# Kernel tuning notes

Hardware: AMD Instinct MI355X
Metric: run time of the kernel (lower is better)

Reference implementation:

```python
import jax, jax.numpy as jnp
import numpy as np

N_NODES = 50000


def gcn_conv(x, edge_index, W, b, n_nodes):
    # Linear transform first (as in PyG GCNConv), then normalized aggregation
    xw = x @ W  # [N, out]
    src, dst = edge_index[0], edge_index[1]
    loops = jnp.arange(n_nodes, dtype=src.dtype)
    s = jnp.concatenate([src, loops])  # add self-loops
    d = jnp.concatenate([dst, loops])
    deg = jax.ops.segment_sum(jnp.ones_like(s, dtype=xw.dtype), d, num_segments=n_nodes)
    dinv = jnp.where(deg > 0, jax.lax.rsqrt(deg), 0.0)
    norm = dinv[s] * dinv[d]  # [E+N]
    msg = xw[s] * norm[:, None]  # gather + scale
    out = jax.ops.segment_sum(msg, d, num_segments=n_nodes)  # scatter-add
    return out + b


def setup_inputs() -> dict:
    key = jax.random.key(0)
    k1, k2, k3, k4 = jax.random.split(key, 4)
    in_dim, hidden = 128, 128
    n_edges = 625000
    x = jax.random.normal(k1, (N_NODES, in_dim), dtype=jnp.float32)
    edge_index = jax.random.randint(k2, (2, n_edges), 0, N_NODES, dtype=jnp.int64)
    # glorot-ish scale
    W1 = jax.random.normal(k3, (in_dim, hidden), dtype=jnp.float32) * (1.0 / np.sqrt(in_dim))
    b1 = jnp.zeros((hidden,), dtype=jnp.float32)
    W2 = jax.random.normal(k4, (hidden, hidden), dtype=jnp.float32) * (1.0 / np.sqrt(hidden))
    b2 = jnp.zeros((hidden,), dtype=jnp.float32)
    return {"x": x, "edge_index": edge_index, "W1": W1, "b1": b1, "W2": W2, "b2": b2}


def reference(x, edge_index, W1, b1, W2, b2):
    n = x.shape[0]
    h = gcn_conv(x, edge_index, W1, b1, n)
    h = jax.nn.relu(h)
    # dropout(p=0.3) is identity in eval mode
    h = gcn_conv(h, edge_index, W2, b2, n)
    return jax.nn.relu(h)
```

## Files before the change

### kernel.cpp

```cpp
#include <hip/hip_runtime.h>
#include <hip/hip_bf16.h>

#define NNODES 50000
#define BKT 64
#define LP 136
#define EPT 8
#define AGG_BLOCKS 2048
#define AGE_BLOCKS 512

typedef short bf16x8 __attribute__((ext_vector_type(8)));
typedef float f32x4 __attribute__((ext_vector_type(4)));

__device__ __forceinline__ unsigned short f2bf_rn(float f) {
    unsigned int u = __float_as_uint(f);
    return (unsigned short)((u + 0x7fffu + ((u >> 16) & 1u)) >> 16);
}
__device__ __forceinline__ float bf_lo(unsigned int u) { return __uint_as_float(u << 16); }
__device__ __forceinline__ float bf_hi(unsigned int u) { return __uint_as_float(u & 0xffff0000u); }


__global__ __launch_bounds__(256) void k_wt(const float* __restrict__ W1,
                                            const float* __restrict__ W2,
                                            unsigned short* __restrict__ WT1,
                                            unsigned short* __restrict__ WT2,
                                            int* __restrict__ cnt, int N) {
    __shared__ float tile[128 * 129];
    int b = blockIdx.x, t = threadIdx.x;
    if (b < 2) {
        const float* W = b ? W2 : W1;
        unsigned short* WT = b ? WT2 : WT1;
        for (int idx = t; idx < 128 * 128; idx += 256)
            tile[(idx >> 7) * 129 + (idx & 127)] = W[idx];
        __syncthreads();
        for (int idx = t; idx < 128 * 128; idx += 256) {
            int c = idx >> 7, k = idx & 127;
            WT[c * 128 + k] = f2bf_rn(tile[k * 129 + c]);
        }
    } else {
        int i = (b - 2) * 256 + t;
        if (i < N) cnt[i] = 0;
    }
}


__device__ __forceinline__ void gather_accum(const unsigned int* __restrict__ xwb,
                                             const int* __restrict__ cnt,
                                             const unsigned short* __restrict__ bp,
                                             int degc, int lane,
                                             float& ax, float& ay) {
    float px = 0.f, py = 0.f;
    int j = 0;
    for (; j + 8 <= degc; j += 8) {
        int4 q = *(const int4*)&bp[j];
        int s0 = q.x & 0xffff, s1 = (int)((unsigned)q.x >> 16);
        int s2 = q.y & 0xffff, s3 = (int)((unsigned)q.y >> 16);
        int s4 = q.z & 0xffff, s5 = (int)((unsigned)q.z >> 16);
        int s6 = q.w & 0xffff, s7 = (int)((unsigned)q.w >> 16);
        unsigned int u0 = xwb[(size_t)s0 * 64 + lane];
        unsigned int u1 = xwb[(size_t)s1 * 64 + lane];
        unsigned int u2 = xwb[(size_t)s2 * 64 + lane];
        unsigned int u3 = xwb[(size_t)s3 * 64 + lane];
        unsigned int u4 = xwb[(size_t)s4 * 64 + lane];
        unsigned int u5 = xwb[(size_t)s5 * 64 + lane];
        unsigned int u6 = xwb[(size_t)s6 * 64 + lane];
        unsigned int u7 = xwb[(size_t)s7 * 64 + lane];
        float w0 = rsqrtf((float)cnt[s0] + 1.0f), w1 = rsqrtf((float)cnt[s1] + 1.0f);
        float w2 = rsqrtf((float)cnt[s2] + 1.0f), w3 = rsqrtf((float)cnt[s3] + 1.0f);
        float w4 = rsqrtf((float)cnt[s4] + 1.0f), w5 = rsqrtf((float)cnt[s5] + 1.0f);
        float w6 = rsqrtf((float)cnt[s6] + 1.0f), w7 = rsqrtf((float)cnt[s7] + 1.0f);
        ax = fmaf(bf_lo(u0), w0, ax);  ay = fmaf(bf_hi(u0), w0, ay);
        px = fmaf(bf_lo(u1), w1, px);  py = fmaf(bf_hi(u1), w1, py);
        ax = fmaf(bf_lo(u2), w2, ax);  ay = fmaf(bf_hi(u2), w2, ay);
        px = fmaf(bf_lo(u3), w3, px);  py = fmaf(bf_hi(u3), w3, py);
        ax = fmaf(bf_lo(u4), w4, ax);  ay = fmaf(bf_hi(u4), w4, ay);
        px = fmaf(bf_lo(u5), w5, px);  py = fmaf(bf_hi(u5), w5, py);
        ax = fmaf(bf_lo(u6), w6, ax);  ay = fmaf(bf_hi(u6), w6, ay);
        px = fmaf(bf_lo(u7), w7, px);  py = fmaf(bf_hi(u7), w7, py);
    }
    if (j + 4 <= degc) {
        int2 q = *(const int2*)&bp[j];
        int s0 = q.x & 0xffff, s1 = (int)((unsigned)q.x >> 16);
        int s2 = q.y & 0xffff, s3 = (int)((unsigned)q.y >> 16);
        unsigned int u0 = xwb[(size_t)s0 * 64 + lane];
        unsigned int u1 = xwb[(size_t)s1 * 64 + lane];
        unsigned int u2 = xwb[(size_t)s2 * 64 + lane];
        unsigned int u3 = xwb[(size_t)s3 * 64 + lane];
        float w0 = rsqrtf((float)cnt[s0] + 1.0f), w1 = rsqrtf((float)cnt[s1] + 1.0f);
        float w2 = rsqrtf((float)cnt[s2] + 1.0f), w3 = rsqrtf((float)cnt[s3] + 1.0f);
        ax = fmaf(bf_lo(u0), w0, ax);  ay = fmaf(bf_hi(u0), w0, ay);
        px = fmaf(bf_lo(u1), w1, px);  py = fmaf(bf_hi(u1), w1, py);
        ax = fmaf(bf_lo(u2), w2, ax);  ay = fmaf(bf_hi(u2), w2, ay);
        px = fmaf(bf_lo(u3), w3, px);  py = fmaf(bf_hi(u3), w3, py);
        j += 4;
    }
    for (; j < degc; ++j) {
        int s = bp[j];
        float wv = rsqrtf((float)cnt[s] + 1.0f);
        unsigned int u = xwb[(size_t)s * 64 + lane];
        ax = fmaf(bf_lo(u), wv, ax);
        ay = fmaf(bf_hi(u), wv, ay);
    }
    ax += px;
    ay += py;
}


__device__ __forceinline__ void gather_sum(const unsigned int* __restrict__ xwb,
                                           const unsigned short* __restrict__ bp,
                                           int degc, int lane,
                                           float& ax, float& ay) {
    float px = 0.f, py = 0.f;
    int j = 0;
    for (; j + 8 <= degc; j += 8) {
        int4 q = *(const int4*)&bp[j];
        int s0 = q.x & 0xffff, s1 = (int)((unsigned)q.x >> 16);
        int s2 = q.y & 0xffff, s3 = (int)((unsigned)q.y >> 16);
        int s4 = q.z & 0xffff, s5 = (int)((unsigned)q.z >> 16);
        int s6 = q.w & 0xffff, s7 = (int)((unsigned)q.w >> 16);
        unsigned int u0 = xwb[(size_t)s0 * 64 + lane];
        unsigned int u1 = xwb[(size_t)s1 * 64 + lane];
        unsigned int u2 = xwb[(size_t)s2 * 64 + lane];
        unsigned int u3 = xwb[(size_t)s3 * 64 + lane];
        unsigned int u4 = xwb[(size_t)s4 * 64 + lane];
        unsigned int u5 = xwb[(size_t)s5 * 64 + lane];
        unsigned int u6 = xwb[(size_t)s6 * 64 + lane];
        unsigned int u7 = xwb[(size_t)s7 * 64 + lane];
        ax += bf_lo(u0);  ay += bf_hi(u0);
        px += bf_lo(u1);  py += bf_hi(u1);
        ax += bf_lo(u2);  ay += bf_hi(u2);
        px += bf_lo(u3);  py += bf_hi(u3);
        ax += bf_lo(u4);  ay += bf_hi(u4);
        px += bf_lo(u5);  py += bf_hi(u5);
        ax += bf_lo(u6);  ay += bf_hi(u6);
        px += bf_lo(u7);  py += bf_hi(u7);
    }
    if (j + 4 <= degc) {
        int2 q = *(const int2*)&bp[j];
        int s0 = q.x & 0xffff, s1 = (int)((unsigned)q.x >> 16);
        int s2 = q.y & 0xffff, s3 = (int)((unsigned)q.y >> 16);
        unsigned int u0 = xwb[(size_t)s0 * 64 + lane];
        unsigned int u1 = xwb[(size_t)s1 * 64 + lane];
        unsigned int u2 = xwb[(size_t)s2 * 64 + lane];
        unsigned int u3 = xwb[(size_t)s3 * 64 + lane];
        ax += bf_lo(u0);  ay += bf_hi(u0);
        px += bf_lo(u1);  py += bf_hi(u1);
        ax += bf_lo(u2);  ay += bf_hi(u2);
        px += bf_lo(u3);  py += bf_hi(u3);
        j += 4;
    }
    for (; j < degc; ++j) {
        int s = bp[j];
        unsigned int u = xwb[(size_t)s * 64 + lane];
        ax += bf_lo(u);
        ay += bf_hi(u);
    }
    ax += px;
    ay += py;
}


__global__ __launch_bounds__(256) void k_gemmbucket(const float* __restrict__ X,
                                                    const unsigned short* __restrict__ WT,
                                                    unsigned short* __restrict__ Yb, int n,
                                                    const int* __restrict__ src,
                                                    const int* __restrict__ dst,
                                                    int* __restrict__ cnt,
                                                    unsigned short* __restrict__ bkt,
                                                    int E, int EB8) {
    __shared__ unsigned short Ep[64 * LP];
    int t = threadIdx.x;
    int b = blockIdx.x;
    int region = EB8 * 3;
    if (b < region && (b % 3) == 0) {
        int bid = b / 3;
        int e0 = bid * 256 * EPT + t * EPT;
        if (e0 + EPT <= E) {
            int4 sa = *(const int4*)&src[e0];
            int4 sb = *(const int4*)&src[e0 + 4];
            int4 da = *(const int4*)&dst[e0];
            int4 db = *(const int4*)&dst[e0 + 4];
            int p;
            p = atomicAdd(&cnt[da.x], 1); if (p < BKT) bkt[(size_t)da.x * BKT + p] = (unsigned short)sa.x;
            p = atomicAdd(&cnt[da.y], 1); if (p < BKT) bkt[(size_t)da.y * BKT + p] = (unsigned short)sa.y;
            p = atomicAdd(&cnt[da.z], 1); if (p < BKT) bkt[(size_t)da.z * BKT + p] = (unsigned short)sa.z;
            p = atomicAdd(&cnt[da.w], 1); if (p < BKT) bkt[(size_t)da.w * BKT + p] = (unsigned short)sa.w;
            p = atomicAdd(&cnt[db.x], 1); if (p < BKT) bkt[(size_t)db.x * BKT + p] = (unsigned short)sb.x;
            p = atomicAdd(&cnt[db.y], 1); if (p < BKT) bkt[(size_t)db.y * BKT + p] = (unsigned short)sb.y;
            p = atomicAdd(&cnt[db.z], 1); if (p < BKT) bkt[(size_t)db.z * BKT + p] = (unsigned short)sb.z;
            p = atomicAdd(&cnt[db.w], 1); if (p < BKT) bkt[(size_t)db.w * BKT + p] = (unsigned short)sb.w;
        } else {
#pragma unroll
            for (int k = 0; k < EPT; ++k) {
                int e = e0 + k;
                if (e < E) {
                    int s = src[e], d = dst[e];
                    int pos = atomicAdd(&cnt[d], 1);
                    if (pos < BKT) bkt[(size_t)d * BKT + pos] = (unsigned short)s;
                }
            }
        }
        return;
    }
    int gb = (b < region) ? (b - (b + 2) / 3) : (b - EB8);
    int lane = t & 63, w = t >> 6;
    int m = lane & 15, quad = lane >> 4;
    int base = gb * 64 + w * 16;
    int row = min(base + m, n - 1);

    bf16x8 a[4];
#pragma unroll
    for (int kt = 0; kt < 4; ++kt) {
        const float* pa = &X[(size_t)row * 128 + kt * 32 + quad * 8];
        float4 v0 = *(const float4*)pa;
        float4 v1 = *(const float4*)(pa + 4);
        a[kt][0] = (short)f2bf_rn(v0.x); a[kt][1] = (short)f2bf_rn(v0.y);
        a[kt][2] = (short)f2bf_rn(v0.z); a[kt][3] = (short)f2bf_rn(v0.w);
        a[kt][4] = (short)f2bf_rn(v1.x); a[kt][5] = (short)f2bf_rn(v1.y);
        a[kt][6] = (short)f2bf_rn(v1.z); a[kt][7] = (short)f2bf_rn(v1.w);
    }

    f32x4 acc[8];
#pragma unroll
    for (int i = 0; i < 8; ++i) acc[i] = f32x4{0.f, 0.f, 0.f, 0.f};
#pragma unroll
    for (int kt = 0; kt < 4; ++kt) {
        int ko = kt * 32 + quad * 8;
#pragma unroll
        for (int ct = 0; ct < 8; ++ct) {
            bf16x8 bfrag = *(const bf16x8*)&WT[(ct * 16 + m) * 128 + ko];
            acc[ct] = __builtin_amdgcn_mfma_f32_16x16x32_bf16(a[kt], bfrag, acc[ct], 0, 0, 0);
        }
    }

    unsigned short* ep = &Ep[w * 16 * LP];
#pragma unroll
    for (int ct = 0; ct < 8; ++ct)
#pragma unroll
        for (int r = 0; r < 4; ++r)
            ep[(quad * 4 + r) * LP + ct * 16 + m] = f2bf_rn(acc[ct][r]);
    __syncthreads();
    int rr = lane & 15, cc = lane >> 4;
    int orow = base + rr;
    if (orow < n) {
#pragma unroll
        for (int i2 = 0; i2 < 4; ++i2)
            ((uint4*)&Yb[(size_t)orow * 128])[cc * 4 + i2] =
                *(const uint4*)&ep[rr * LP + (cc * 4 + i2) * 8];
    }
}


__global__ __launch_bounds__(1024, 2) void k_aggemm(const unsigned int* __restrict__ xw1,
                                                    const int* __restrict__ cnt,
                                                    const unsigned short* __restrict__ bkt,
                                                    const float* __restrict__ bias,
                                                    const unsigned short* __restrict__ WT2,
                                                    unsigned short* __restrict__ xw2,
                                                    int n, int ntiles) {
    __shared__ unsigned short At[16 * LP];
    __shared__ float dis[16];
    int t = threadIdx.x, lane = t & 63, w = t >> 6;
    int m = lane & 15, quad = lane >> 4;
    float bx = bias[lane * 2], by = bias[lane * 2 + 1];

    for (int tile = blockIdx.x; tile < ntiles; tile += gridDim.x) {
        int base = tile * 16;
        int i = min(base + w, n - 1);
        int deg = cnt[i];
        int degc = min(deg, BKT);
        float di = rsqrtf((float)deg + 1.0f);
        unsigned int v0 = xw1[(size_t)i * 64 + lane];
        float ax = di * bf_lo(v0), ay = di * bf_hi(v0);
        gather_accum(xw1, cnt, &bkt[(size_t)i * BKT], degc, lane, ax, ay);
        ax = fmaxf(fmaf(di, ax, bx), 0.0f);
        ay = fmaxf(fmaf(di, ay, by), 0.0f);
        ((unsigned int*)&At[w * LP])[lane] =
            (unsigned)f2bf_rn(ax) | ((unsigned)f2bf_rn(ay) << 16);
        if (lane == 0) dis[w] = di;
        __syncthreads();

        f32x4 acc = f32x4{0.f, 0.f, 0.f, 0.f};
        if (w < 8) {
            bf16x8 a[4];
#pragma unroll
            for (int kt = 0; kt < 4; ++kt)
                a[kt] = *(const bf16x8*)&At[m * LP + kt * 32 + quad * 8];
#pragma unroll
            for (int kt = 0; kt < 4; ++kt) {
                bf16x8 bfrag = *(const bf16x8*)&WT2[(w * 16 + m) * 128 + kt * 32 + quad * 8];
                acc = __builtin_amdgcn_mfma_f32_16x16x32_bf16(a[kt], bfrag, acc, 0, 0, 0);
            }
        }
        __syncthreads();
        if (w < 8) {
#pragma unroll
            for (int r = 0; r < 4; ++r)
                At[(quad * 4 + r) * LP + w * 16 + m] = f2bf_rn(acc[r] * dis[quad * 4 + r]);
        }
        __syncthreads();
        if (t < 256) {
            int row = t >> 4, q = t & 15;
            int orow = base + row;
            if (orow < n)
                *(uint4*)&xw2[(size_t)orow * 128 + q * 8] =
                    *(const uint4*)&At[row * LP + q * 8];
        }
        __syncthreads();
    }
}


__global__ __launch_bounds__(256) void k_agg(const unsigned int* __restrict__ xwb,
                                             const int* __restrict__ cnt,
                                             const unsigned short* __restrict__ bkt,
                                             const float* __restrict__ bias,
                                             float* __restrict__ out, int n) {
    int lane = threadIdx.x & 63;
    int gw = (blockIdx.x * 256 + threadIdx.x) >> 6;
    int nw = (gridDim.x * 256) >> 6;
    float bx = bias[lane * 2], by = bias[lane * 2 + 1];
    for (int i = gw; i < n; i += nw) {
        int deg = cnt[i];
        int degc = min(deg, BKT);
        float di = rsqrtf((float)deg + 1.0f);
        unsigned int v0 = xwb[(size_t)i * 64 + lane];
        float ax = bf_lo(v0), ay = bf_hi(v0);
        gather_sum(xwb, &bkt[(size_t)i * BKT], degc, lane, ax, ay);
        ax = fmaxf(fmaf(di, ax, bx), 0.0f);
        ay = fmaxf(fmaf(di, ay, by), 0.0f);
        ((float2*)out)[(size_t)i * 64 + lane] = make_float2(ax, ay);
    }
}


extern "C" void kernel_launch(void* const* d_in, const int* in_sizes, int n_in,
                              void* d_out, int out_size, void* d_ws, size_t ws_size,
                              hipStream_t stream) {
    const float* x  = (const float*)d_in[0];
    const int*   ei = (const int*)d_in[1];
    const float* W1 = (const float*)d_in[2];
    const float* b1 = (const float*)d_in[3];
    const float* W2 = (const float*)d_in[4];
    const float* b2 = (const float*)d_in[5];
    float* out = (float*)d_out;

    const int N = NNODES;
    const int E = in_sizes[1] / 2;
    const int* src = ei;
    const int* dst = ei + E;

    char* p = (char*)d_ws;
    size_t off = 0;
    auto take = [&](size_t bytes) -> void* {
        void* r = p + off;
        off = (off + bytes + 255) & ~(size_t)255;
        return r;
    };
    int* cnt = (int*)take((size_t)N * 4);
    unsigned short* bkt = (unsigned short*)take((size_t)N * BKT * 2);
    unsigned short* w1t = (unsigned short*)take(128 * 128 * 2);
    unsigned short* w2t = (unsigned short*)take(128 * 128 * 2);
    unsigned short* xw1 = (unsigned short*)take((size_t)N * 128 * 2);
    unsigned short* xw2 = (unsigned short*)take((size_t)N * 128 * 2);

    const int NB = (N + 255) / 256;
    const int EB8 = (E + 256 * EPT - 1) / (256 * EPT);
    const int GB = (N + 63) / 64;
    const int NT = (N + 15) / 16;

    k_wt<<<2 + NB, 256, 0, stream>>>(W1, W2, w1t, w2t, cnt, N);
    k_gemmbucket<<<EB8 + GB, 256, 0, stream>>>(x, w1t, xw1, N, src, dst, cnt, bkt, E, EB8);
    k_aggemm<<<AGE_BLOCKS, 1024, 0, stream>>>((const unsigned int*)xw1, cnt, bkt,
                                              b1, w2t, xw2, N, NT);
    k_agg<<<AGG_BLOCKS, 256, 0, stream>>>((const unsigned int*)xw2, cnt, bkt,
                                          b2, out, N);
}
```

Measured before the change: 219.4 us.

## Restructure fused aggregate-GEMM to per-wave 16-row tiles with LDS-staged W2

The fused layer-1 aggregation plus layer-2 GEMM kernel now has each wave aggregate 16 nodes into its own LDS tile, then run a full 16x128 MFMA product against W2, which is staged once per block in LDS. Before, a 1024-thread persistent block synchronised three times per 16-node tile, left half its waves idle during the GEMM, and read W2 fragments from global memory. The new layout drops all block-wide barriers in the main loop and raises MFMA work per wave. In exchange it uses about 52KB of LDS per block, which may limit occupancy, and holds more accumulator registers.

```diff
diff --git a/kernel.cpp b/kernel.cpp
--- a/kernel.cpp
+++ b/kernel.cpp
@@ -6,7 +6,6 @@
 #define LP 136
 #define EPT 8
 #define AGG_BLOCKS 2048
-#define AGE_BLOCKS 512
 
 typedef short bf16x8 __attribute__((ext_vector_type(8)));
 typedef float f32x4 __attribute__((ext_vector_type(4)));
@@ -250,22 +249,30 @@
 }
 
 
-__global__ __launch_bounds__(1024, 2) void k_aggemm(const unsigned int* __restrict__ xw1,
-                                                    const int* __restrict__ cnt,
-                                                    const unsigned short* __restrict__ bkt,
-                                                    const float* __restrict__ bias,
-                                                    const unsigned short* __restrict__ WT2,
-                                                    unsigned short* __restrict__ xw2,
-                                                    int n, int ntiles) {
-    __shared__ unsigned short At[16 * LP];
-    __shared__ float dis[16];
+__global__ __launch_bounds__(256) void k_aggemm(const unsigned int* __restrict__ xw1,
+                                                const int* __restrict__ cnt,
+                                                const unsigned short* __restrict__ bkt,
+                                                const float* __restrict__ bias,
+                                                const unsigned short* __restrict__ WT2,
+                                                unsigned short* __restrict__ xw2, int n) {
+    __shared__ unsigned short Wl[128 * LP];
+    __shared__ unsigned short At[4 * 16 * LP];
+    __shared__ float dsw[4][16];
     int t = threadIdx.x, lane = t & 63, w = t >> 6;
     int m = lane & 15, quad = lane >> 4;
+
+    for (int idx = t; idx < 128 * 16; idx += 256) {
+        int r = idx >> 4, c8 = (idx & 15) << 3;
+        *(uint4*)&Wl[r * LP + c8] = *(const uint4*)&WT2[r * 128 + c8];
+    }
     float bx = bias[lane * 2], by = bias[lane * 2 + 1];
-
-    for (int tile = blockIdx.x; tile < ntiles; tile += gridDim.x) {
-        int base = tile * 16;
-        int i = min(base + w, n - 1);
+    __syncthreads();
+
+    unsigned short* Aw = &At[w * 16 * LP];
+    int base = blockIdx.x * 64 + w * 16;
+
+    for (int nd = 0; nd < 16; ++nd) {
+        int i = min(base + nd, n - 1);
         int deg = cnt[i];
         int degc = min(deg, BKT);
         float di = rsqrtf((float)deg + 1.0f);
@@ -274,38 +281,43 @@
         gather_accum(xw1, cnt, &bkt[(size_t)i * BKT], degc, lane, ax, ay);
         ax = fmaxf(fmaf(di, ax, bx), 0.0f);
         ay = fmaxf(fmaf(di, ay, by), 0.0f);
-        ((unsigned int*)&At[w * LP])[lane] =
+        ((unsigned int*)&Aw[nd * LP])[lane] =
             (unsigned)f2bf_rn(ax) | ((unsigned)f2bf_rn(ay) << 16);
-        if (lane == 0) dis[w] = di;
-        __syncthreads();
-
-        f32x4 acc = f32x4{0.f, 0.f, 0.f, 0.f};
-        if (w < 8) {
-            bf16x8 a[4];
-#pragma unroll
-            for (int kt = 0; kt < 4; ++kt)
-                a[kt] = *(const bf16x8*)&At[m * LP + kt * 32 + quad * 8];
-#pragma unroll
-            for (int kt = 0; kt < 4; ++kt) {
-                bf16x8 bfrag = *(const bf16x8*)&WT2[(w * 16 + m) * 128 + kt * 32 + quad * 8];
-                acc = __builtin_amdgcn_mfma_f32_16x16x32_bf16(a[kt], bfrag, acc, 0, 0, 0);
-            }
+        if (lane == 0) dsw[w][nd] = di;
+    }
+
+    bf16x8 a[4];
+#pragma unroll
+    for (int kt = 0; kt < 4; ++kt)
+        a[kt] = *(const bf16x8*)&Aw[m * LP + kt * 32 + quad * 8];
+    f32x4 acc[8];
+#pragma unroll
+    for (int i = 0; i < 8; ++i) acc[i] = f32x4{0.f, 0.f, 0.f, 0.f};
+#pragma unroll
+    for (int kt = 0; kt < 4; ++kt) {
+        int ko = kt * 32 + quad * 8;
+#pragma unroll
+        for (int ct = 0; ct < 8; ++ct) {
+            bf16x8 bfrag = *(const bf16x8*)&Wl[(ct * 16 + m) * LP + ko];
+            acc[ct] = __builtin_amdgcn_mfma_f32_16x16x32_bf16(a[kt], bfrag, acc[ct], 0, 0, 0);
         }
-        __syncthreads();
-        if (w < 8) {
-#pragma unroll
-            for (int r = 0; r < 4; ++r)
-                At[(quad * 4 + r) * LP + w * 16 + m] = f2bf_rn(acc[r] * dis[quad * 4 + r]);
-        }
-        __syncthreads();
-        if (t < 256) {
-            int row = t >> 4, q = t & 15;
-            int orow = base + row;
-            if (orow < n)
-                *(uint4*)&xw2[(size_t)orow * 128 + q * 8] =
-                    *(const uint4*)&At[row * LP + q * 8];
-        }
-        __syncthreads();
+    }
+
+    float dr[4];
+#pragma unroll
+    for (int r = 0; r < 4; ++r) dr[r] = dsw[w][quad * 4 + r];
+#pragma unroll
+    for (int ct = 0; ct < 8; ++ct)
+#pragma unroll
+        for (int r = 0; r < 4; ++r)
+            Aw[(quad * 4 + r) * LP + ct * 16 + m] = f2bf_rn(acc[ct][r] * dr[r]);
+    int rr = lane & 15, cc = lane >> 4;
+    int orow = base + rr;
+    if (orow < n) {
+#pragma unroll
+        for (int i2 = 0; i2 < 4; ++i2)
+            ((uint4*)&xw2[(size_t)orow * 128])[cc * 4 + i2] =
+                *(const uint4*)&Aw[rr * LP + (cc * 4 + i2) * 8];
     }
 }
 
@@ -366,12 +378,10 @@
     const int NB = (N + 255) / 256;
     const int EB8 = (E + 256 * EPT - 1) / (256 * EPT);
     const int GB = (N + 63) / 64;
-    const int NT = (N + 15) / 16;
 
     k_wt<<<2 + NB, 256, 0, stream>>>(W1, W2, w1t, w2t, cnt, N);
     k_gemmbucket<<<EB8 + GB, 256, 0, stream>>>(x, w1t, xw1, N, src, dst, cnt, bkt, E, EB8);
-    k_aggemm<<<AGE_BLOCKS, 1024, 0, stream>>>((const unsigned int*)xw1, cnt, bkt,
-                                              b1, w2t, xw2, N, NT);
+    k_aggemm<<<GB, 256, 0, stream>>>((const unsigned int*)xw1, cnt, bkt, b1, w2t, xw2, N);
     k_agg<<<AGG_BLOCKS, 256, 0, stream>>>((const unsigned int*)xw2, cnt, bkt,
                                           b2, out, N);
 }
```

Measured after the change: 243.1 us. +10.8%, slower.

## Precompute degree normalisation and retile fused aggregate-GEMM to 64-node blocks

Applied to the files above, without the earlier changes.

Adds a small kernel that precomputes dinv = rsqrt(deg+1) once per node, so the gather loops load a float instead of doing a count load plus rsqrt for every neighbour. The fused layer-1 aggregation and layer-2 GEMM kernel is changed from a grid-stride loop over 16-node tiles to one 64-node tile per block. Each wave now aggregates four nodes, W2 is staged once into LDS, and every wave issues two MFMAs per k-step. This removes per-tile barriers and the repeated global reads of W2 fragments, at the cost of an extra launch, more LDS per block, and a larger grid.

```diff
diff --git a/kernel.cpp b/kernel.cpp
--- a/kernel.cpp
+++ b/kernel.cpp
@@ -6,7 +6,6 @@
 #define LP 136
 #define EPT 8
 #define AGG_BLOCKS 2048
-#define AGE_BLOCKS 512
 
 typedef short bf16x8 __attribute__((ext_vector_type(8)));
 typedef float f32x4 __attribute__((ext_vector_type(4)));
@@ -43,11 +42,11 @@
 }
 
 
-__device__ __forceinline__ void gather_accum(const unsigned int* __restrict__ xwb,
-                                             const int* __restrict__ cnt,
-                                             const unsigned short* __restrict__ bp,
-                                             int degc, int lane,
-                                             float& ax, float& ay) {
+__device__ __forceinline__ void gather_wsum(const unsigned int* __restrict__ xwb,
+                                            const float* __restrict__ dinv,
+                                            const unsigned short* __restrict__ bp,
+                                            int degc, int lane,
+                                            float& ax, float& ay) {
     float px = 0.f, py = 0.f;
     int j = 0;
     for (; j + 8 <= degc; j += 8) {
@@ -64,10 +63,8 @@
         unsigned int u5 = xwb[(size_t)s5 * 64 + lane];
         unsigned int u6 = xwb[(size_t)s6 * 64 + lane];
         unsigned int u7 = xwb[(size_t)s7 * 64 + lane];
-        float w0 = rsqrtf((float)cnt[s0] + 1.0f), w1 = rsqrtf((float)cnt[s1] + 1.0f);
-        float w2 = rsqrtf((float)cnt[s2] + 1.0f), w3 = rsqrtf((float)cnt[s3] + 1.0f);
-        float w4 = rsqrtf((float)cnt[s4] + 1.0f), w5 = rsqrtf((float)cnt[s5] + 1.0f);
-        float w6 = rsqrtf((float)cnt[s6] + 1.0f), w7 = rsqrtf((float)cnt[s7] + 1.0f);
+        float w0 = dinv[s0], w1 = dinv[s1], w2 = dinv[s2], w3 = dinv[s3];
+        float w4 = dinv[s4], w5 = dinv[s5], w6 = dinv[s6], w7 = dinv[s7];
         ax = fmaf(bf_lo(u0), w0, ax);  ay = fmaf(bf_hi(u0), w0, ay);
         px = fmaf(bf_lo(u1), w1, px);  py = fmaf(bf_hi(u1), w1, py);
         ax = fmaf(bf_lo(u2), w2, ax);  ay = fmaf(bf_hi(u2), w2, ay);
@@ -85,8 +82,7 @@
         unsigned int u1 = xwb[(size_t)s1 * 64 + lane];
         unsigned int u2 = xwb[(size_t)s2 * 64 + lane];
         unsigned int u3 = xwb[(size_t)s3 * 64 + lane];
-        float w0 = rsqrtf((float)cnt[s0] + 1.0f), w1 = rsqrtf((float)cnt[s1] + 1.0f);
-        float w2 = rsqrtf((float)cnt[s2] + 1.0f), w3 = rsqrtf((float)cnt[s3] + 1.0f);
+        float w0 = dinv[s0], w1 = dinv[s1], w2 = dinv[s2], w3 = dinv[s3];
         ax = fmaf(bf_lo(u0), w0, ax);  ay = fmaf(bf_hi(u0), w0, ay);
         px = fmaf(bf_lo(u1), w1, px);  py = fmaf(bf_hi(u1), w1, py);
         ax = fmaf(bf_lo(u2), w2, ax);  ay = fmaf(bf_hi(u2), w2, ay);
@@ -95,7 +91,7 @@
     }
     for (; j < degc; ++j) {
         int s = bp[j];
-        float wv = rsqrtf((float)cnt[s] + 1.0f);
+        float wv = dinv[s];
         unsigned int u = xwb[(size_t)s * 64 + lane];
         ax = fmaf(bf_lo(u), wv, ax);
         ay = fmaf(bf_hi(u), wv, ay);
@@ -250,69 +246,84 @@
 }
 
 
-__global__ __launch_bounds__(1024, 2) void k_aggemm(const unsigned int* __restrict__ xw1,
+__global__ __launch_bounds__(256) void k_dinv(const int* __restrict__ cnt,
+                                              float* __restrict__ dinv, int N) {
+    int i = blockIdx.x * 256 + threadIdx.x;
+    if (i < N) dinv[i] = rsqrtf((float)cnt[i] + 1.0f);
+}
+
+
+__global__ __launch_bounds__(1024, 8) void k_aggemm(const unsigned int* __restrict__ xw1,
                                                     const int* __restrict__ cnt,
                                                     const unsigned short* __restrict__ bkt,
+                                                    const float* __restrict__ dinv,
                                                     const float* __restrict__ bias,
                                                     const unsigned short* __restrict__ WT2,
-                                                    unsigned short* __restrict__ xw2,
-                                                    int n, int ntiles) {
-    __shared__ unsigned short At[16 * LP];
-    __shared__ float dis[16];
+                                                    unsigned short* __restrict__ xw2, int n) {
+    __shared__ unsigned short Wl[128 * LP];
+    __shared__ unsigned short At[64 * LP];
+    __shared__ float dsw[64];
     int t = threadIdx.x, lane = t & 63, w = t >> 6;
     int m = lane & 15, quad = lane >> 4;
+    int base = blockIdx.x * 64;
+
+    for (int idx = t; idx < 128 * 16; idx += 1024) {
+        int r = idx >> 4, c8 = (idx & 15) << 3;
+        *(uint4*)&Wl[r * LP + c8] = *(const uint4*)&WT2[r * 128 + c8];
+    }
     float bx = bias[lane * 2], by = bias[lane * 2 + 1];
 
-    for (int tile = blockIdx.x; tile < ntiles; tile += gridDim.x) {
-        int base = tile * 16;
-        int i = min(base + w, n - 1);
-        int deg = cnt[i];
-        int degc = min(deg, BKT);
-        float di = rsqrtf((float)deg + 1.0f);
+#pragma unroll
+    for (int k = 0; k < 4; ++k) {
+        int nd = w * 4 + k;
+        int i = min(base + nd, n - 1);
+        int degc = min(cnt[i], BKT);
+        float di = dinv[i];
         unsigned int v0 = xw1[(size_t)i * 64 + lane];
         float ax = di * bf_lo(v0), ay = di * bf_hi(v0);
-        gather_accum(xw1, cnt, &bkt[(size_t)i * BKT], degc, lane, ax, ay);
+        gather_wsum(xw1, dinv, &bkt[(size_t)i * BKT], degc, lane, ax, ay);
         ax = fmaxf(fmaf(di, ax, bx), 0.0f);
         ay = fmaxf(fmaf(di, ay, by), 0.0f);
-        ((unsigned int*)&At[w * LP])[lane] =
+        ((unsigned int*)&At[nd * LP])[lane] =
             (unsigned)f2bf_rn(ax) | ((unsigned)f2bf_rn(ay) << 16);
-        if (lane == 0) dis[w] = di;
-        __syncthreads();
-
-        f32x4 acc = f32x4{0.f, 0.f, 0.f, 0.f};
-        if (w < 8) {
-            bf16x8 a[4];
-#pragma unroll
-            for (int kt = 0; kt < 4; ++kt)
-                a[kt] = *(const bf16x8*)&At[m * LP + kt * 32 + quad * 8];
-#pragma unroll
-            for (int kt = 0; kt < 4; ++kt) {
-                bf16x8 bfrag = *(const bf16x8*)&WT2[(w * 16 + m) * 128 + kt * 32 + quad * 8];
-                acc = __builtin_amdgcn_mfma_f32_16x16x32_bf16(a[kt], bfrag, acc, 0, 0, 0);
-            }
-        }
-        __syncthreads();
-        if (w < 8) {
-#pragma unroll
-            for (int r = 0; r < 4; ++r)
-                At[(quad * 4 + r) * LP + w * 16 + m] = f2bf_rn(acc[r] * dis[quad * 4 + r]);
-        }
-        __syncthreads();
-        if (t < 256) {
-            int row = t >> 4, q = t & 15;
-            int orow = base + row;
-            if (orow < n)
-                *(uint4*)&xw2[(size_t)orow * 128 + q * 8] =
-                    *(const uint4*)&At[row * LP + q * 8];
-        }
-        __syncthreads();
-    }
+        if (lane == 0) dsw[nd] = di;
+    }
+    __syncthreads();
+
+    int ct = w & 7, rb = w >> 3;
+    f32x4 acc0 = f32x4{0.f, 0.f, 0.f, 0.f};
+    f32x4 acc1 = f32x4{0.f, 0.f, 0.f, 0.f};
+#pragma unroll
+    for (int kt = 0; kt < 4; ++kt) {
+        int ko = kt * 32 + quad * 8;
+        bf16x8 bfrag = *(const bf16x8*)&Wl[(ct * 16 + m) * LP + ko];
+        bf16x8 a0 = *(const bf16x8*)&At[(rb * 16 + m) * LP + ko];
+        bf16x8 a1 = *(const bf16x8*)&At[((rb + 2) * 16 + m) * LP + ko];
+        acc0 = __builtin_amdgcn_mfma_f32_16x16x32_bf16(a0, bfrag, acc0, 0, 0, 0);
+        acc1 = __builtin_amdgcn_mfma_f32_16x16x32_bf16(a1, bfrag, acc1, 0, 0, 0);
+    }
+    __syncthreads();
+
+#pragma unroll
+    for (int r = 0; r < 4; ++r) {
+        int r0 = rb * 16 + quad * 4 + r;
+        int r1 = (rb + 2) * 16 + quad * 4 + r;
+        At[r0 * LP + ct * 16 + m] = f2bf_rn(acc0[r] * dsw[r0]);
+        At[r1 * LP + ct * 16 + m] = f2bf_rn(acc1[r] * dsw[r1]);
+    }
+    __syncthreads();
+
+    int row = t >> 4, q = t & 15;
+    int orow = base + row;
+    if (orow < n)
+        *(uint4*)&xw2[(size_t)orow * 128 + q * 8] = *(const uint4*)&At[row * LP + q * 8];
 }
 
 
 __global__ __launch_bounds__(256) void k_agg(const unsigned int* __restrict__ xwb,
                                              const int* __restrict__ cnt,
                                              const unsigned short* __restrict__ bkt,
+                                             const float* __restrict__ dinv,
                                              const float* __restrict__ bias,
                                              float* __restrict__ out, int n) {
     int lane = threadIdx.x & 63;
@@ -320,9 +331,8 @@
     int nw = (gridDim.x * 256) >> 6;
     float bx = bias[lane * 2], by = bias[lane * 2 + 1];
     for (int i = gw; i < n; i += nw) {
-        int deg = cnt[i];
-        int degc = min(deg, BKT);
-        float di = rsqrtf((float)deg + 1.0f);
+        int degc = min(cnt[i], BKT);
+        float di = dinv[i];
         unsigned int v0 = xwb[(size_t)i * 64 + lane];
         float ax = bf_lo(v0), ay = bf_hi(v0);
         gather_sum(xwb, &bkt[(size_t)i * BKT], degc, lane, ax, ay);
@@ -362,16 +372,17 @@
     unsigned short* w2t = (unsigned short*)take(128 * 128 * 2);
     unsigned short* xw1 = (unsigned short*)take((size_t)N * 128 * 2);
     unsigned short* xw2 = (unsigned short*)take((size_t)N * 128 * 2);
+    float* dinv = (float*)take((size_t)N * 4);
 
     const int NB = (N + 255) / 256;
     const int EB8 = (E + 256 * EPT - 1) / (256 * EPT);
     const int GB = (N + 63) / 64;
-    const int NT = (N + 15) / 16;
 
     k_wt<<<2 + NB, 256, 0, stream>>>(W1, W2, w1t, w2t, cnt, N);
     k_gemmbucket<<<EB8 + GB, 256, 0, stream>>>(x, w1t, xw1, N, src, dst, cnt, bkt, E, EB8);
-    k_aggemm<<<AGE_BLOCKS, 1024, 0, stream>>>((const unsigned int*)xw1, cnt, bkt,
-                                              b1, w2t, xw2, N, NT);
-    k_agg<<<AGG_BLOCKS, 256, 0, stream>>>((const unsigned int*)xw2, cnt, bkt,
+    k_dinv<<<NB, 256, 0, stream>>>(cnt, dinv, N);
+    k_aggemm<<<GB, 1024, 0, stream>>>((const unsigned int*)xw1, cnt, bkt, dinv,
+                                      b1, w2t, xw2, N);
+    k_agg<<<AGG_BLOCKS, 256, 0, stream>>>((const unsigned int*)xw2, cnt, bkt, dinv,
                                           b2, out, N);
 }
```

Result: faster. 192.7 us (-12.2%).
